# Performance work log

Measured on AMD Instinct MI355X. Metric: run time of the kernel, lower is better.

The kernel has to match this reference:

```python
import jax, jax.numpy as jnp
import numpy as np

N = 50000      # nodes
E = 800000     # edges (avg degree 16)
F_IN = 3       # dataset.num_node_features
H = 256        # hidden_channels
G = 64         # batch_size (num graphs)
OUT = 24       # lin_out output dim


def setup_inputs() -> dict:
    key = jax.random.key(0)
    ks = jax.random.split(key, 16)
    s = 0.05
    inp = {
        "x": jax.random.normal(ks[0], (N, F_IN), jnp.float32),
        "edge_index": jax.random.randint(ks[1], (2, E), 0, N, dtype=jnp.int32),
        "batch": jnp.sort(jax.random.randint(ks[2], (N,), 0, G, dtype=jnp.int32)),
        # layer 1 (F_IN -> H)
        "w_rel1": jax.random.normal(ks[3], (F_IN, H), jnp.float32) * s,
        "w_root1": jax.random.normal(ks[4], (F_IN, H), jnp.float32) * s,
        "b1": jnp.zeros((H,), jnp.float32),
        # layers 2..7 (H -> H), stacked
        "w_rel": jax.random.normal(ks[5], (6, H, H), jnp.float32) * s,
        "w_root": jax.random.normal(ks[6], (6, H, H), jnp.float32) * s,
        "b": jnp.zeros((6, H), jnp.float32),
        # output head
        "w_out": jax.random.normal(ks[7], (H, OUT), jnp.float32) * s,
        "b_out": jnp.zeros((OUT,), jnp.float32),
    }
    return inp


def reference(x, edge_index, batch, w_rel1, w_root1, b1, w_rel, w_root, b, w_out, b_out):
    src, dst = edge_index[0], edge_index[1]

    def conv(h, wr, wro, bb):
        # PyG GraphConv with add aggregation:
        # out_i = W_rel @ sum_{j -> i} h_j + b + W_root @ h_i
        agg = jax.ops.segment_sum(h[src], dst, num_segments=N)
        return agg @ wr + h @ wro + bb

    h = jax.nn.relu(conv(x, w_rel1, w_root1, b1))
    for i in range(6):
        h = jax.nn.relu(conv(h, w_rel[i], w_root[i], b[i]))

    # global_mean_pool over batch segment ids
    counts = jax.ops.segment_sum(jnp.ones((N,), h.dtype), batch, num_segments=G)
    pooled = jax.ops.segment_sum(h, batch, num_segments=G) / jnp.maximum(counts, 1.0)[:, None]

    # dropout is identity in eval mode
    return pooled @ w_out + b_out
```

## Files before the change

kernel.cpp:

```cpp
#include <hip/hip_runtime.h>

#define N_NODES 50000
#define MPAD 50048
#define N_EDGES 800000
#define H 256
#define K_CAT 512
#define G_BATCH 64
#define OUT_DIM 24

#define SCAN_BLK 256
#define NBLK ((N_NODES + SCAN_BLK - 1) / SCAN_BLK)

typedef __attribute__((ext_vector_type(8))) short short8;
typedef __attribute__((ext_vector_type(4))) float float4v;

__device__ __forceinline__ float bf2f(unsigned short u) {
    return __uint_as_float(((unsigned)u) << 16);
}
__device__ __forceinline__ unsigned short f2bf(float f) {
    unsigned x = __float_as_uint(f);
    unsigned r = (x + 0x7FFFu + ((x >> 16) & 1u)) >> 16;
    return (unsigned short)r;
}

__device__ __forceinline__ void async_copy16(void* lds, const void* g) {
    __builtin_amdgcn_global_load_lds(
        (const __attribute__((address_space(1))) unsigned int*)g,
        (__attribute__((address_space(3))) unsigned int*)lds, 16, 0, 0);
}



__global__ void histo_kernel(const int* __restrict__ dst, int* __restrict__ deg,
                             int* __restrict__ epos) {
    int e = blockIdx.x * blockDim.x + threadIdx.x;
    if (e < N_EDGES) epos[e] = atomicAdd(&deg[dst[e]], 1);
}

__global__ void scan_block(const int* __restrict__ deg, int* __restrict__ rowptr,
                           int* __restrict__ blockSums) {
    __shared__ int s[SCAN_BLK];
    int idx = blockIdx.x * SCAN_BLK + threadIdx.x;
    int v = (idx < N_NODES) ? deg[idx] : 0;
    s[threadIdx.x] = v;
    __syncthreads();
    for (int off = 1; off < SCAN_BLK; off <<= 1) {
        int t = (threadIdx.x >= off) ? s[threadIdx.x - off] : 0;
        __syncthreads();
        s[threadIdx.x] += t;
        __syncthreads();
    }
    if (idx < N_NODES) rowptr[idx] = s[threadIdx.x] - v;
    if (threadIdx.x == SCAN_BLK - 1) blockSums[blockIdx.x] = s[threadIdx.x];
}

__global__ void scan_finish(int* __restrict__ rowptr, const int* __restrict__ blockSums) {
    __shared__ int s[SCAN_BLK];
    int t = threadIdx.x;
    int v = (t < NBLK) ? blockSums[t] : 0;
    s[t] = v;
    __syncthreads();
    for (int off = 1; off < SCAN_BLK; off <<= 1) {
        int tv = (t >= off) ? s[t - off] : 0;
        __syncthreads();
        s[t] += tv;
        __syncthreads();
    }
    int prefix = (blockIdx.x > 0) ? s[blockIdx.x - 1] : 0;
    int idx = blockIdx.x * SCAN_BLK + t;
    if (idx < N_NODES) rowptr[idx] += prefix;
    if (blockIdx.x == 0 && t == 0) rowptr[N_NODES] = s[NBLK - 1];
}

__global__ void fill_csr(const int* __restrict__ src, const int* __restrict__ dst,
                         const int* __restrict__ rowptr, const int* __restrict__ epos,
                         int* __restrict__ csr_src) {
    int e = blockIdx.x * blockDim.x + threadIdx.x;
    if (e >= N_EDGES) return;
    csr_src[rowptr[dst[e]] + epos[e]] = src[e];
}


__global__ void prep_weights(const float* __restrict__ w_rel, const float* __restrict__ w_root,
                             unsigned short* __restrict__ WcatT) {
    int idx = blockIdx.x * blockDim.x + threadIdx.x;
    if (idx >= 6 * K_CAT * H) return;
    int n = idx & (H - 1);
    int k = (idx >> 8) & (K_CAT - 1);
    int l = idx >> 17;
    float v;
    if (k < H) {
        int f = (k & 0xC0) | ((k & 3) << 4) | ((k >> 2) & 15);
        v = w_rel[(size_t)l * H * H + f * H + n];
    } else {
        v = w_root[(size_t)l * H * H + (k - H) * H + n];
    }
    WcatT[(size_t)l * H * K_CAT + (size_t)n * K_CAT + k] = f2bf(v);
}


__global__ void agg3(const float* __restrict__ x, const int* __restrict__ rowptr,
                     const int* __restrict__ csr_src, float* __restrict__ agg) {
    int n = blockIdx.x * blockDim.x + threadIdx.x;
    if (n >= N_NODES) return;
    int beg = rowptr[n], end = rowptr[n + 1];
    float a0 = 0.f, a1 = 0.f, a2 = 0.f;
    for (int i = beg; i < end; ++i) {
        int s = csr_src[i];
        a0 += x[s * 3 + 0];
        a1 += x[s * 3 + 1];
        a2 += x[s * 3 + 2];
    }
    agg[n * 3 + 0] = a0;
    agg[n * 3 + 1] = a1;
    agg[n * 3 + 2] = a2;
}

__global__ void layer1_kernel(const float* __restrict__ x, const float* __restrict__ agg,
                              const float* __restrict__ wr, const float* __restrict__ wro,
                              const float* __restrict__ bias, unsigned short* __restrict__ cat,
                              unsigned char* __restrict__ h8, float* __restrict__ hscale) {
    __shared__ unsigned char tmp[H];
    int n = blockIdx.x;
    int f = threadIdx.x;
    float a0 = agg[n * 3 + 0], a1 = agg[n * 3 + 1], a2 = agg[n * 3 + 2];
    float x0 = x[n * 3 + 0], x1 = x[n * 3 + 1], x2 = x[n * 3 + 2];
    float v = bias[f];
    v += a0 * wr[0 * H + f] + a1 * wr[1 * H + f] + a2 * wr[2 * H + f];
    v += x0 * wro[0 * H + f] + x1 * wro[1 * H + f] + x2 * wro[2 * H + f];
    v = fmaxf(v, 0.f);
    cat[(size_t)n * K_CAT + H + f] = f2bf(v);
    float m = v;
#pragma unroll
    for (int off = 1; off < 64; off <<= 1) m = fmaxf(m, __shfl_xor(m, off, 64));
    float inv = m > 0.f ? 255.f / m : 0.f;
    tmp[(f & 0xC0) | ((f & 15) << 2) | ((f >> 4) & 3)] = (unsigned char)(v * inv + 0.5f);
    if ((f & 63) == 0) hscale[n * 4 + (f >> 6)] = m * (1.f / 255.f);
    __syncthreads();
    if (f < 64) *(unsigned*)(h8 + (size_t)n * H + f * 4) = *(const unsigned*)(tmp + f * 4);
}


__global__ __launch_bounds__(256) void aggH(unsigned short* __restrict__ cat,
                                            const unsigned char* __restrict__ h8,
                                            const float* __restrict__ hscale,
                                            const int* __restrict__ rowptr,
                                            const int* __restrict__ csr_src) {
    int gtid = blockIdx.x * blockDim.x + threadIdx.x;
    int node = gtid >> 6;
    if (node >= N_NODES) return;
    int lane = threadIdx.x & 63;
    int sub = lane >> 4;
    int fl = lane & 15;
    int g = fl >> 2;
    int beg = rowptr[node], end = rowptr[node + 1];

    if (beg >= end) {
        if (sub == 0) {
            uint4 z = make_uint4(0, 0, 0, 0);
            unsigned short* o = cat + (size_t)node * K_CAT + fl * 16;
            *(uint4*)o = z;
            *(uint4*)(o + 8) = z;
        }
        return;
    }

    float acc[16] = {};
    const unsigned char* base = h8 + fl * 16;
    int last = end - 1;

    int ia = beg + sub;
    int ca = ia < end ? ia : last;
    int sa = csr_src[ca];
    int ib = beg + 4 + sub;
    int cb = ib < end ? ib : last;
    int sb = csr_src[cb];
    float sca = (ia < end) ? hscale[sa * 4 + g] : 0.f;
    uint4 qa = *(const uint4*)(base + (size_t)sa * H);

    for (int i = beg; i < end; i += 4) {
        int ic = i + 8 + sub;
        int cc = ic < end ? ic : last;
        int sn = csr_src[cc];
        int inb = i + 4 + sub;
        float scb = (inb < end) ? hscale[sb * 4 + g] : 0.f;
        uint4 qb = *(const uint4*)(base + (size_t)sb * H);

        float sc = sca;
        acc[0]  = fmaf((float)(qa.x & 0xffu), sc, acc[0]);
        acc[1]  = fmaf((float)((qa.x >> 8) & 0xffu), sc, acc[1]);
        acc[2]  = fmaf((float)((qa.x >> 16) & 0xffu), sc, acc[2]);
        acc[3]  = fmaf((float)(qa.x >> 24), sc, acc[3]);
        acc[4]  = fmaf((float)(qa.y & 0xffu), sc, acc[4]);
        acc[5]  = fmaf((float)((qa.y >> 8) & 0xffu), sc, acc[5]);
        acc[6]  = fmaf((float)((qa.y >> 16) & 0xffu), sc, acc[6]);
        acc[7]  = fmaf((float)(qa.y >> 24), sc, acc[7]);
        acc[8]  = fmaf((float)(qa.z & 0xffu), sc, acc[8]);
        acc[9]  = fmaf((float)((qa.z >> 8) & 0xffu), sc, acc[9]);
        acc[10] = fmaf((float)((qa.z >> 16) & 0xffu), sc, acc[10]);
        acc[11] = fmaf((float)(qa.z >> 24), sc, acc[11]);
        acc[12] = fmaf((float)(qa.w & 0xffu), sc, acc[12]);
        acc[13] = fmaf((float)((qa.w >> 8) & 0xffu), sc, acc[13]);
        acc[14] = fmaf((float)((qa.w >> 16) & 0xffu), sc, acc[14]);
        acc[15] = fmaf((float)(qa.w >> 24), sc, acc[15]);

        sa = sb; sb = sn; sca = scb; qa = qb;
    }

#pragma unroll
    for (int j = 0; j < 16; j++) {
        acc[j] += __shfl_xor(acc[j], 16, 64);
        acc[j] += __shfl_xor(acc[j], 32, 64);
    }

    if (sub == 0) {
        unsigned short* o = cat + (size_t)node * K_CAT + fl * 16;
        uint4 p0, p1;
        p0.x = (unsigned)f2bf(acc[0])  | ((unsigned)f2bf(acc[1]) << 16);
        p0.y = (unsigned)f2bf(acc[2])  | ((unsigned)f2bf(acc[3]) << 16);
        p0.z = (unsigned)f2bf(acc[4])  | ((unsigned)f2bf(acc[5]) << 16);
        p0.w = (unsigned)f2bf(acc[6])  | ((unsigned)f2bf(acc[7]) << 16);
        p1.x = (unsigned)f2bf(acc[8])  | ((unsigned)f2bf(acc[9]) << 16);
        p1.y = (unsigned)f2bf(acc[10]) | ((unsigned)f2bf(acc[11]) << 16);
        p1.z = (unsigned)f2bf(acc[12]) | ((unsigned)f2bf(acc[13]) << 16);
        p1.w = (unsigned)f2bf(acc[14]) | ((unsigned)f2bf(acc[15]) << 16);
        *(uint4*)o = p0;
        *(uint4*)(o + 8) = p1;
    }
}


#define GBM 64
#define GBN 128
#define GBK 64

__global__ __launch_bounds__(256) void gemm_mfma(
    const unsigned short* __restrict__ cat, const unsigned short* __restrict__ WcatT,
    const float* __restrict__ bias, unsigned short* __restrict__ catOut,
    unsigned char* __restrict__ h8, float* __restrict__ hscale) {
    __shared__ unsigned short sA[GBM][GBK];
    __shared__ unsigned short sB[GBN][GBK];

    const int tid = threadIdx.x;
    const int wave = tid >> 6;
    const int lane = tid & 63;
    const int quad = lane >> 4;
    const int l16 = lane & 15;
    const int wm0 = (wave & 1) * 32;
    const int wn0 = (wave >> 1) * 64;
    const int m0 = blockIdx.x * GBM;
    const int n0 = blockIdx.y * GBN;

    const int rowoff = lane >> 3;
    const int schunk = ((lane & 7) ^ rowoff) * 8;
    const unsigned short* Asrc[2];
    const unsigned short* Bsrc[4];
#pragma unroll
    for (int j = 0; j < 2; j++) {
        int q = wave * 2 + j;
        Asrc[j] = cat + (size_t)(m0 + q * 8 + rowoff) * K_CAT + schunk;
    }
#pragma unroll
    for (int j = 0; j < 4; j++) {
        int q = wave * 4 + j;
        Bsrc[j] = WcatT + (size_t)(n0 + q * 8 + rowoff) * K_CAT + schunk;
    }

    const int sw = l16 & 7;
    const int ca0 = (quad ^ sw) * 8;
    const int ca1 = ((4 + quad) ^ sw) * 8;

    float4v acc[2][4] = {};

    for (int kk = 0; kk < K_CAT; kk += GBK) {
#pragma unroll
        for (int j = 0; j < 2; j++)
            async_copy16((char*)sA + (wave * 2 + j) * 1024, Asrc[j] + kk);
#pragma unroll
        for (int j = 0; j < 4; j++)
            async_copy16((char*)sB + (wave * 4 + j) * 1024, Bsrc[j] + kk);
        __syncthreads();

        short8 a[2][2], b[4][2];
#pragma unroll
        for (int i = 0; i < 2; i++) {
            const unsigned short* ra = &sA[wm0 + i * 16 + l16][0];
            a[i][0] = *(const short8*)(ra + ca0);
            a[i][1] = *(const short8*)(ra + ca1);
        }
#pragma unroll
        for (int i = 0; i < 4; i++) {
            const unsigned short* rb = &sB[wn0 + i * 16 + l16][0];
            b[i][0] = *(const short8*)(rb + ca0);
            b[i][1] = *(const short8*)(rb + ca1);
        }
#pragma unroll
        for (int sub = 0; sub < 2; sub++)
#pragma unroll
            for (int mi = 0; mi < 2; mi++)
#pragma unroll
                for (int ni = 0; ni < 4; ni++)
                    acc[mi][ni] = __builtin_amdgcn_mfma_f32_16x16x32_bf16(
                        a[mi][sub], b[ni][sub], acc[mi][ni], 0, 0, 0);
        __syncthreads();
    }

    const int hb = n0 + wn0 + l16 * 4;
    const int gsc = (n0 + wn0) >> 6;
    float bcol[4];
#pragma unroll
    for (int ni = 0; ni < 4; ni++) bcol[ni] = bias[n0 + wn0 + ni * 16 + l16];

#pragma unroll
    for (int mi = 0; mi < 2; mi++) {
        int rowb = m0 + wm0 + mi * 16 + quad * 4;
#pragma unroll
        for (int r = 0; r < 4; r++) {
            int row = rowb + r;
            float v0 = fmaxf(acc[mi][0][r] + bcol[0], 0.f);
            float v1 = fmaxf(acc[mi][1][r] + bcol[1], 0.f);
            float v2 = fmaxf(acc[mi][2][r] + bcol[2], 0.f);
            float v3 = fmaxf(acc[mi][3][r] + bcol[3], 0.f);
            unsigned short* co = catOut + (size_t)row * K_CAT + H + n0 + wn0 + l16;
            co[0]  = f2bf(v0);
            co[16] = f2bf(v1);
            co[32] = f2bf(v2);
            co[48] = f2bf(v3);
            float m = fmaxf(fmaxf(v0, v1), fmaxf(v2, v3));
            m = fmaxf(m, __shfl_xor(m, 1, 64));
            m = fmaxf(m, __shfl_xor(m, 2, 64));
            m = fmaxf(m, __shfl_xor(m, 4, 64));
            m = fmaxf(m, __shfl_xor(m, 8, 64));
            float inv = m > 0.f ? 255.f / m : 0.f;
            unsigned p = (unsigned)(v0 * inv + 0.5f)
                       | ((unsigned)(v1 * inv + 0.5f) << 8)
                       | ((unsigned)(v2 * inv + 0.5f) << 16)
                       | ((unsigned)(v3 * inv + 0.5f) << 24);
            *(unsigned*)(h8 + (size_t)row * H + hb) = p;
            if (l16 == 0) hscale[row * 4 + gsc] = m * (1.f / 255.f);
        }
    }
}


__device__ __forceinline__ int lowerBound(const int* __restrict__ batch, int val) {
    int lo = 0, hi = N_NODES;
    while (lo < hi) {
        int mid = (lo + hi) >> 1;
        if (batch[mid] < val) lo = mid + 1; else hi = mid;
    }
    return lo;
}

__global__ void pool_partial(const unsigned short* __restrict__ cat, const int* __restrict__ batch,
                             float* __restrict__ pooled) {
    int g = blockIdx.x;
    int seg = blockIdx.y;
    int f = threadIdx.x;
    int start = lowerBound(batch, g);
    int end = lowerBound(batch, g + 1);
    int len = end - start;
    int s0 = start + (int)((long long)len * seg / 8);
    int s1 = start + (int)((long long)len * (seg + 1) / 8);
    float sum = 0.f;
    for (int n = s0; n < s1; ++n)
        sum += bf2f(cat[(size_t)n * K_CAT + H + f]);
    if (s1 > s0)
        atomicAdd(&pooled[g * H + f], sum);
}

__global__ void head_kernel(const float* __restrict__ pooled, const int* __restrict__ batch,
                            const float* __restrict__ w_out, const float* __restrict__ b_out,
                            float* __restrict__ out) {
    int g = blockIdx.x;
    int o = threadIdx.x;
    int start = lowerBound(batch, g);
    int end = lowerBound(batch, g + 1);
    float cnt = fmaxf((float)(end - start), 1.f);
    float sum = 0.f;
    for (int f = 0; f < H; ++f)
        sum += pooled[g * H + f] * w_out[f * OUT_DIM + o];
    out[g * OUT_DIM + o] = b_out[o] + sum / cnt;
}


extern "C" void kernel_launch(void* const* d_in, const int* in_sizes, int n_in,
                              void* d_out, int out_size, void* d_ws, size_t ws_size,
                              hipStream_t stream) {
    const float* x      = (const float*)d_in[0];
    const int*   ei     = (const int*)d_in[1];
    const int*   batch  = (const int*)d_in[2];
    const float* w_rel1 = (const float*)d_in[3];
    const float* w_root1= (const float*)d_in[4];
    const float* b1     = (const float*)d_in[5];
    const float* w_rel  = (const float*)d_in[6];
    const float* w_root = (const float*)d_in[7];
    const float* b      = (const float*)d_in[8];
    const float* w_out  = (const float*)d_in[9];
    const float* b_out  = (const float*)d_in[10];
    float* out = (float*)d_out;

    const int* src = ei;
    const int* dst = ei + N_EDGES;

    unsigned short* catA  = (unsigned short*)d_ws;
    unsigned short* catB  = catA + (size_t)MPAD * K_CAT;
    unsigned short* WcatT = catB + (size_t)MPAD * K_CAT;
    float* agg3buf = (float*)(WcatT + (size_t)6 * H * K_CAT);
    float* pooled  = agg3buf + (size_t)N_NODES * 4;
    float* hscale  = pooled + G_BATCH * H;
    int* rowptr    = (int*)(hscale + (size_t)MPAD * 4);
    int* degcur    = rowptr + (N_NODES + 1);
    int* blockSums = degcur + N_NODES;
    int* csr_src   = blockSums + SCAN_BLK;
    int* epos      = csr_src + N_EDGES;
    unsigned char* h8 = (unsigned char*)(epos + N_EDGES);

    hipMemsetAsync(degcur, 0, N_NODES * sizeof(int), stream);
    histo_kernel<<<(N_EDGES + 255) / 256, 256, 0, stream>>>(dst, degcur, epos);
    scan_block<<<NBLK, SCAN_BLK, 0, stream>>>(degcur, rowptr, blockSums);
    scan_finish<<<NBLK, SCAN_BLK, 0, stream>>>(rowptr, blockSums);
    fill_csr<<<(N_EDGES + 255) / 256, 256, 0, stream>>>(src, dst, rowptr, epos, csr_src);

    prep_weights<<<(6 * K_CAT * H + 255) / 256, 256, 0, stream>>>(w_rel, w_root, WcatT);

    agg3<<<(N_NODES + 255) / 256, 256, 0, stream>>>(x, rowptr, csr_src, agg3buf);
    layer1_kernel<<<N_NODES, H, 0, stream>>>(x, agg3buf, w_rel1, w_root1, b1, catA, h8, hscale);

    unsigned short* cur = catA;
    unsigned short* nxt = catB;
    for (int l = 0; l < 6; ++l) {
        aggH<<<(N_NODES * 64 + 255) / 256, 256, 0, stream>>>(cur, h8, hscale, rowptr, csr_src);
        dim3 grid(MPAD / GBM, H / GBN);
        gemm_mfma<<<grid, 256, 0, stream>>>(cur, WcatT + (size_t)l * H * K_CAT,
                                            b + (size_t)l * H, nxt, h8, hscale);
        unsigned short* t = cur; cur = nxt; nxt = t;
    }

    hipMemsetAsync(pooled, 0, G_BATCH * H * sizeof(float), stream);
    pool_partial<<<dim3(G_BATCH, 8), 256, 0, stream>>>(cur, batch, pooled);
    head_kernel<<<G_BATCH, OUT_DIM, 0, stream>>>(pooled, batch, w_out, b_out, out);
}
```

Measured before the change: 655.7 us.

## Pad CSR rows to multiples of four and split aggH by feature slice

Each node's CSR row is padded to a multiple of four edges. The padding slots point at a dummy zero node at index MPAD, whose h8 row and scales are zeroed, so the per-edge bounds checks in aggH go away. aggH is restructured so that each block handles 4 nodes for one 64-feature slice (N_NODES blocks), and each lane loads 4 bytes instead of 16. This spreads the gather over more waves and cuts register pressure, at the cost of more index and scale loads per feature and one extra pad_fill kernel.

```diff
diff --git a/kernel.cpp b/kernel.cpp
--- a/kernel.cpp
+++ b/kernel.cpp
@@ -41,7 +41,7 @@
                            int* __restrict__ blockSums) {
     __shared__ int s[SCAN_BLK];
     int idx = blockIdx.x * SCAN_BLK + threadIdx.x;
-    int v = (idx < N_NODES) ? deg[idx] : 0;
+    int v = (idx < N_NODES) ? ((deg[idx] + 3) & ~3) : 0;
     s[threadIdx.x] = v;
     __syncthreads();
     for (int off = 1; off < SCAN_BLK; off <<= 1) {
@@ -74,10 +74,23 @@
 
 __global__ void fill_csr(const int* __restrict__ src, const int* __restrict__ dst,
                          const int* __restrict__ rowptr, const int* __restrict__ epos,
-                         int* __restrict__ csr_src) {
+                         int* __restrict__ csr_src, unsigned char* __restrict__ h8,
+                         float* __restrict__ hscale) {
     int e = blockIdx.x * blockDim.x + threadIdx.x;
+    if (e < 64) ((unsigned*)(h8 + (size_t)MPAD * H))[e] = 0u;
+    if (e >= 64 && e < 68) hscale[(size_t)MPAD * 4 + (e - 64)] = 0.f;
     if (e >= N_EDGES) return;
     csr_src[rowptr[dst[e]] + epos[e]] = src[e];
+}
+
+__global__ void pad_fill(const int* __restrict__ rowptr, const int* __restrict__ deg,
+                         int* __restrict__ csr_src) {
+    int n = blockIdx.x * blockDim.x + threadIdx.x;
+    if (n >= N_NODES) return;
+    int d = deg[n];
+    int e0 = rowptr[n] + d;
+    int e1 = rowptr[n] + ((d + 3) & ~3);
+    for (int i = e0; i < e1; ++i) csr_src[i] = MPAD;
 }
 
 
@@ -100,10 +113,11 @@
 
 
 __global__ void agg3(const float* __restrict__ x, const int* __restrict__ rowptr,
-                     const int* __restrict__ csr_src, float* __restrict__ agg) {
+                     const int* __restrict__ deg, const int* __restrict__ csr_src,
+                     float* __restrict__ agg) {
     int n = blockIdx.x * blockDim.x + threadIdx.x;
     if (n >= N_NODES) return;
-    int beg = rowptr[n], end = rowptr[n + 1];
+    int beg = rowptr[n], end = beg + deg[n];
     float a0 = 0.f, a1 = 0.f, a2 = 0.f;
     for (int i = beg; i < end; ++i) {
         int s = csr_src[i];
@@ -146,86 +160,50 @@
                                             const float* __restrict__ hscale,
                                             const int* __restrict__ rowptr,
                                             const int* __restrict__ csr_src) {
-    int gtid = blockIdx.x * blockDim.x + threadIdx.x;
-    int node = gtid >> 6;
-    if (node >= N_NODES) return;
-    int lane = threadIdx.x & 63;
-    int sub = lane >> 4;
-    int fl = lane & 15;
-    int g = fl >> 2;
-    int beg = rowptr[node], end = rowptr[node + 1];
-
-    if (beg >= end) {
-        if (sub == 0) {
-            uint4 z = make_uint4(0, 0, 0, 0);
-            unsigned short* o = cat + (size_t)node * K_CAT + fl * 16;
-            *(uint4*)o = z;
-            *(uint4*)(o + 8) = z;
+    const int slice = blockIdx.x & 3;
+    const int node = (blockIdx.x >> 2) * 4 + (threadIdx.x >> 6);
+    const int lane = threadIdx.x & 63;
+    const int sub = lane >> 4;
+    const int fl = lane & 15;
+    const int beg = rowptr[node];
+    const int n_it = (rowptr[node + 1] - beg) >> 2;
+
+    float a0 = 0.f, a1 = 0.f, a2 = 0.f, a3 = 0.f;
+    const unsigned char* base = h8 + slice * 64 + fl * 4;
+    const float* hs = hscale + slice;
+    const int* ip = csr_src + beg + sub;
+
+    if (n_it > 0) {
+        int i1 = ip[0];
+        int i2 = (n_it > 1) ? ip[4] : MPAD;
+        float sc = hs[i1 * 4];
+        unsigned q = *(const unsigned*)(base + (size_t)i1 * H);
+        for (int t = 1; t < n_it; ++t) {
+            int i3 = (t + 1 < n_it) ? ip[(t + 1) * 4] : MPAD;
+            float sc2 = hs[i2 * 4];
+            unsigned q2 = *(const unsigned*)(base + (size_t)i2 * H);
+            a0 = fmaf((float)(q & 0xffu), sc, a0);
+            a1 = fmaf((float)((q >> 8) & 0xffu), sc, a1);
+            a2 = fmaf((float)((q >> 16) & 0xffu), sc, a2);
+            a3 = fmaf((float)(q >> 24), sc, a3);
+            q = q2; sc = sc2; i2 = i3;
         }
-        return;
-    }
-
-    float acc[16] = {};
-    const unsigned char* base = h8 + fl * 16;
-    int last = end - 1;
-
-    int ia = beg + sub;
-    int ca = ia < end ? ia : last;
-    int sa = csr_src[ca];
-    int ib = beg + 4 + sub;
-    int cb = ib < end ? ib : last;
-    int sb = csr_src[cb];
-    float sca = (ia < end) ? hscale[sa * 4 + g] : 0.f;
-    uint4 qa = *(const uint4*)(base + (size_t)sa * H);
-
-    for (int i = beg; i < end; i += 4) {
-        int ic = i + 8 + sub;
-        int cc = ic < end ? ic : last;
-        int sn = csr_src[cc];
-        int inb = i + 4 + sub;
-        float scb = (inb < end) ? hscale[sb * 4 + g] : 0.f;
-        uint4 qb = *(const uint4*)(base + (size_t)sb * H);
-
-        float sc = sca;
-        acc[0]  = fmaf((float)(qa.x & 0xffu), sc, acc[0]);
-        acc[1]  = fmaf((float)((qa.x >> 8) & 0xffu), sc, acc[1]);
-        acc[2]  = fmaf((float)((qa.x >> 16) & 0xffu), sc, acc[2]);
-        acc[3]  = fmaf((float)(qa.x >> 24), sc, acc[3]);
-        acc[4]  = fmaf((float)(qa.y & 0xffu), sc, acc[4]);
-        acc[5]  = fmaf((float)((qa.y >> 8) & 0xffu), sc, acc[5]);
-        acc[6]  = fmaf((float)((qa.y >> 16) & 0xffu), sc, acc[6]);
-        acc[7]  = fmaf((float)(qa.y >> 24), sc, acc[7]);
-        acc[8]  = fmaf((float)(qa.z & 0xffu), sc, acc[8]);
-        acc[9]  = fmaf((float)((qa.z >> 8) & 0xffu), sc, acc[9]);
-        acc[10] = fmaf((float)((qa.z >> 16) & 0xffu), sc, acc[10]);
-        acc[11] = fmaf((float)(qa.z >> 24), sc, acc[11]);
-        acc[12] = fmaf((float)(qa.w & 0xffu), sc, acc[12]);
-        acc[13] = fmaf((float)((qa.w >> 8) & 0xffu), sc, acc[13]);
-        acc[14] = fmaf((float)((qa.w >> 16) & 0xffu), sc, acc[14]);
-        acc[15] = fmaf((float)(qa.w >> 24), sc, acc[15]);
-
-        sa = sb; sb = sn; sca = scb; qa = qb;
-    }
-
-#pragma unroll
-    for (int j = 0; j < 16; j++) {
-        acc[j] += __shfl_xor(acc[j], 16, 64);
-        acc[j] += __shfl_xor(acc[j], 32, 64);
-    }
+        a0 = fmaf((float)(q & 0xffu), sc, a0);
+        a1 = fmaf((float)((q >> 8) & 0xffu), sc, a1);
+        a2 = fmaf((float)((q >> 16) & 0xffu), sc, a2);
+        a3 = fmaf((float)(q >> 24), sc, a3);
+    }
+
+    a0 += __shfl_xor(a0, 16, 64); a0 += __shfl_xor(a0, 32, 64);
+    a1 += __shfl_xor(a1, 16, 64); a1 += __shfl_xor(a1, 32, 64);
+    a2 += __shfl_xor(a2, 16, 64); a2 += __shfl_xor(a2, 32, 64);
+    a3 += __shfl_xor(a3, 16, 64); a3 += __shfl_xor(a3, 32, 64);
 
     if (sub == 0) {
-        unsigned short* o = cat + (size_t)node * K_CAT + fl * 16;
-        uint4 p0, p1;
-        p0.x = (unsigned)f2bf(acc[0])  | ((unsigned)f2bf(acc[1]) << 16);
-        p0.y = (unsigned)f2bf(acc[2])  | ((unsigned)f2bf(acc[3]) << 16);
-        p0.z = (unsigned)f2bf(acc[4])  | ((unsigned)f2bf(acc[5]) << 16);
-        p0.w = (unsigned)f2bf(acc[6])  | ((unsigned)f2bf(acc[7]) << 16);
-        p1.x = (unsigned)f2bf(acc[8])  | ((unsigned)f2bf(acc[9]) << 16);
-        p1.y = (unsigned)f2bf(acc[10]) | ((unsigned)f2bf(acc[11]) << 16);
-        p1.z = (unsigned)f2bf(acc[12]) | ((unsigned)f2bf(acc[13]) << 16);
-        p1.w = (unsigned)f2bf(acc[14]) | ((unsigned)f2bf(acc[15]) << 16);
-        *(uint4*)o = p0;
-        *(uint4*)(o + 8) = p1;
+        uint2 p;
+        p.x = (unsigned)f2bf(a0) | ((unsigned)f2bf(a1) << 16);
+        p.y = (unsigned)f2bf(a2) | ((unsigned)f2bf(a3) << 16);
+        *(uint2*)(cat + (size_t)node * K_CAT + slice * 64 + fl * 4) = p;
     }
 }
 
@@ -409,28 +387,30 @@
     float* agg3buf = (float*)(WcatT + (size_t)6 * H * K_CAT);
     float* pooled  = agg3buf + (size_t)N_NODES * 4;
     float* hscale  = pooled + G_BATCH * H;
-    int* rowptr    = (int*)(hscale + (size_t)MPAD * 4);
+    int* rowptr    = (int*)(hscale + (size_t)MPAD * 4 + 4);
     int* degcur    = rowptr + (N_NODES + 1);
     int* blockSums = degcur + N_NODES;
     int* csr_src   = blockSums + SCAN_BLK;
-    int* epos      = csr_src + N_EDGES;
+    int* epos      = csr_src + (N_EDGES + 3 * N_NODES);
     unsigned char* h8 = (unsigned char*)(epos + N_EDGES);
 
     hipMemsetAsync(degcur, 0, N_NODES * sizeof(int), stream);
     histo_kernel<<<(N_EDGES + 255) / 256, 256, 0, stream>>>(dst, degcur, epos);
     scan_block<<<NBLK, SCAN_BLK, 0, stream>>>(degcur, rowptr, blockSums);
     scan_finish<<<NBLK, SCAN_BLK, 0, stream>>>(rowptr, blockSums);
-    fill_csr<<<(N_EDGES + 255) / 256, 256, 0, stream>>>(src, dst, rowptr, epos, csr_src);
+    fill_csr<<<(N_EDGES + 255) / 256, 256, 0, stream>>>(src, dst, rowptr, epos, csr_src,
+                                                        h8, hscale);
+    pad_fill<<<(N_NODES + 255) / 256, 256, 0, stream>>>(rowptr, degcur, csr_src);
 
     prep_weights<<<(6 * K_CAT * H + 255) / 256, 256, 0, stream>>>(w_rel, w_root, WcatT);
 
-    agg3<<<(N_NODES + 255) / 256, 256, 0, stream>>>(x, rowptr, csr_src, agg3buf);
+    agg3<<<(N_NODES + 255) / 256, 256, 0, stream>>>(x, rowptr, degcur, csr_src, agg3buf);
     layer1_kernel<<<N_NODES, H, 0, stream>>>(x, agg3buf, w_rel1, w_root1, b1, catA, h8, hscale);
 
     unsigned short* cur = catA;
     unsigned short* nxt = catB;
     for (int l = 0; l < 6; ++l) {
-        aggH<<<(N_NODES * 64 + 255) / 256, 256, 0, stream>>>(cur, h8, hscale, rowptr, csr_src);
+        aggH<<<N_NODES, 256, 0, stream>>>(cur, h8, hscale, rowptr, csr_src);
         dim3 grid(MPAD / GBM, H / GBN);
         gemm_mfma<<<grid, 256, 0, stream>>>(cur, WcatT + (size_t)l * H * K_CAT,
                                             b + (size_t)l * H, nxt, h8, hscale);
```

After: 928.3 us. +41.6%, slower.
